# Performance work log

Measured on AMD Instinct MI355X. Metric: run time of the kernel, lower is better.

## Reference

```python
import jax, jax.numpy as jnp
import numpy as np

N_SEGMENTS = 50000  # number of destination nodes (index values in [0, N_SEGMENTS))


def setup_inputs() -> dict:
    key = jax.random.key(0)
    k1, k2 = jax.random.split(key)
    input = jax.random.normal(k1, (1600000, 64), dtype=jnp.float32)
    index = jax.random.randint(k2, (1600000,), 0, N_SEGMENTS, dtype=jnp.int64)
    return {"input": input, "index": index}


def reference(input, index):
    # Sum-aggregate rows of `input` grouped by `index`: out[n] = sum_{e: index[e]==n} input[e]
    # Equivalent to the custom loma_sum_aggr forward (scatter-add segmented reduction).
    return jax.ops.segment_sum(input, index, num_segments=N_SEGMENTS)
```

## Files before the change

kernel.cpp:

```cpp
#include <hip/hip_runtime.h>

#define N_SEGMENTS 50000
#define N_ROWS     1600000
#define N_FEAT     64

__global__ void hist_kernel(const int* __restrict__ idx, int* __restrict__ counts) {
    int i = blockIdx.x * 256 + threadIdx.x;
    if (i < N_ROWS) atomicAdd(&counts[idx[i]], 1);
}

__device__ __forceinline__ int wave_incl_scan(int v) {
    int lane = threadIdx.x & 63;
#pragma unroll
    for (int d = 1; d < 64; d <<= 1) {
        int t = __shfl_up(v, d, 64);
        if (lane >= d) v += t;
    }
    return v;
}

__global__ void scan_kernel(const int* __restrict__ counts,
                            int* __restrict__ seg_start,
                            int* __restrict__ cursor) {
    __shared__ int wave_off[16];
    __shared__ int s_carry;
    const int tid  = threadIdx.x;
    const int lane = tid & 63;
    const int wid  = tid >> 6;
    if (tid == 0) s_carry = 0;
    __syncthreads();

    for (int base = 0; base < N_SEGMENTS; base += 1024) {
        int i = base + tid;
        int v = (i < N_SEGMENTS) ? counts[i] : 0;
        int incl = wave_incl_scan(v);
        if (lane == 63) wave_off[wid] = incl;
        __syncthreads();
        if (wid == 0) {
            int ws    = (lane < 16) ? wave_off[lane] : 0;
            int wincl = wave_incl_scan(ws);
            if (lane < 16) wave_off[lane] = wincl - ws;
        }
        __syncthreads();
        int excl = incl - v + wave_off[wid] + s_carry;
        if (i < N_SEGMENTS) { seg_start[i] = excl; cursor[i] = excl; }
        __syncthreads();
        if (tid == 1023) s_carry = excl + v;
        __syncthreads();
    }
    if (tid == 0) seg_start[N_SEGMENTS] = s_carry;
}

__global__ void scatter_kernel(const int* __restrict__ idx,
                               int* __restrict__ cursor,
                               int* __restrict__ rowids) {
    int i = blockIdx.x * 256 + threadIdx.x;
    if (i < N_ROWS) {
        int s = idx[i];
        int p = atomicAdd(&cursor[s], 1);
        rowids[p] = i;
    }
}

__global__ void __launch_bounds__(256)
reduce_kernel(const float* __restrict__ in,
              const int*   __restrict__ rowids,
              const int*   __restrict__ seg_start,
              float*       __restrict__ out) {
    const int wid  = threadIdx.x >> 6;
    const int lane = threadIdx.x & 63;
    const int seg  = blockIdx.x * 4 + wid;
    if (seg >= N_SEGMENTS) return;

    const int beg = seg_start[seg];
    const int end = seg_start[seg + 1];

    float acc = 0.f;
    int r = beg;
    for (; r + 4 <= end; r += 4) {
        int r0 = rowids[r], r1 = rowids[r + 1], r2 = rowids[r + 2], r3 = rowids[r + 3];
        float v0 = in[(long long)r0 * N_FEAT + lane];
        float v1 = in[(long long)r1 * N_FEAT + lane];
        float v2 = in[(long long)r2 * N_FEAT + lane];
        float v3 = in[(long long)r3 * N_FEAT + lane];
        acc += v0; acc += v1; acc += v2; acc += v3;
    }
    for (; r < end; ++r)
        acc += in[(long long)rowids[r] * N_FEAT + lane];

    out[(long long)seg * N_FEAT + lane] = acc;
}

extern "C" void kernel_launch(void* const* d_in, const int* in_sizes, int n_in,
                              void* d_out, int out_size, void* d_ws, size_t ws_size,
                              hipStream_t stream) {
    const float* in  = (const float*)d_in[0];
    const int*   idx = (const int*)d_in[1];
    float*       out = (float*)d_out;

    int* counts    = (int*)d_ws;
    int* seg_start = counts + 50048;
    int* cursor    = seg_start + 50048;
    int* rowids    = cursor + 50048;

    hipMemsetAsync(counts, 0, N_SEGMENTS * sizeof(int), stream);

    const int ROW_BLOCKS = (N_ROWS + 255) / 256;
    hist_kernel   <<<ROW_BLOCKS, 256, 0, stream>>>(idx, counts);
    scan_kernel   <<<1, 1024, 0, stream>>>(counts, seg_start, cursor);
    scatter_kernel<<<ROW_BLOCKS, 256, 0, stream>>>(idx, cursor, rowids);

    const int SEG_BLOCKS = (N_SEGMENTS + 3) / 4;
    reduce_kernel <<<SEG_BLOCKS, 256, 0, stream>>>(in, rowids, seg_start, out);
}
```

Measured before the change: 786.1 us.

## Parallelize prefix scan across blocks and vectorize segment reduce with float4

Replaces the single-block serial scan over 50000 counts with a three-stage multi-block scan (block sums, mid scan, final offsets). The reduce kernel now has each wave load four rows at once as float4, with 16 lanes per row, and combines the four partial sums with xor shuffles before storing. This targets the serial latency of the scan and the narrow per-lane gather loads, at the cost of two extra kernel launches and more workspace.

```diff
diff --git a/kernel.cpp b/kernel.cpp
--- a/kernel.cpp
+++ b/kernel.cpp
@@ -3,11 +3,7 @@
 #define N_SEGMENTS 50000
 #define N_ROWS     1600000
 #define N_FEAT     64
-
-__global__ void hist_kernel(const int* __restrict__ idx, int* __restrict__ counts) {
-    int i = blockIdx.x * 256 + threadIdx.x;
-    if (i < N_ROWS) atomicAdd(&counts[idx[i]], 1);
-}
+#define SCAN_BLOCKS 196
 
 __device__ __forceinline__ int wave_incl_scan(int v) {
     int lane = threadIdx.x & 63;
@@ -19,36 +15,57 @@
     return v;
 }
 
-__global__ void scan_kernel(const int* __restrict__ counts,
-                            int* __restrict__ seg_start,
-                            int* __restrict__ cursor) {
-    __shared__ int wave_off[16];
-    __shared__ int s_carry;
-    const int tid  = threadIdx.x;
-    const int lane = tid & 63;
-    const int wid  = tid >> 6;
-    if (tid == 0) s_carry = 0;
+__global__ void hist_kernel(const int* __restrict__ idx, int* __restrict__ counts) {
+    int i = blockIdx.x * 256 + threadIdx.x;
+    if (i < N_ROWS) atomicAdd(&counts[idx[i]], 1);
+}
+
+__global__ void scan_sums(const int* __restrict__ counts, int* __restrict__ bsums) {
+    const int lane = threadIdx.x & 63, wid = threadIdx.x >> 6;
+    int i = blockIdx.x * 256 + threadIdx.x;
+    int v = (i < N_SEGMENTS) ? counts[i] : 0;
+#pragma unroll
+    for (int m = 1; m < 64; m <<= 1) v += __shfl_xor(v, m, 64);
+    __shared__ int ws[4];
+    if (lane == 0) ws[wid] = v;
     __syncthreads();
+    if (threadIdx.x == 0) bsums[blockIdx.x] = ws[0] + ws[1] + ws[2] + ws[3];
+}
 
-    for (int base = 0; base < N_SEGMENTS; base += 1024) {
-        int i = base + tid;
-        int v = (i < N_SEGMENTS) ? counts[i] : 0;
-        int incl = wave_incl_scan(v);
-        if (lane == 63) wave_off[wid] = incl;
-        __syncthreads();
-        if (wid == 0) {
-            int ws    = (lane < 16) ? wave_off[lane] : 0;
-            int wincl = wave_incl_scan(ws);
-            if (lane < 16) wave_off[lane] = wincl - ws;
-        }
-        __syncthreads();
-        int excl = incl - v + wave_off[wid] + s_carry;
-        if (i < N_SEGMENTS) { seg_start[i] = excl; cursor[i] = excl; }
-        __syncthreads();
-        if (tid == 1023) s_carry = excl + v;
-        __syncthreads();
+__global__ void scan_mid(const int* __restrict__ bsums, int* __restrict__ boffs) {
+    const int tid = threadIdx.x, lane = tid & 63, wid = tid >> 6;
+    __shared__ int ws[4];
+    int v = (tid < SCAN_BLOCKS) ? bsums[tid] : 0;
+    int incl = wave_incl_scan(v);
+    if (lane == 63) ws[wid] = incl;
+    __syncthreads();
+    if (wid == 0) {
+        int s = (lane < 4) ? ws[lane] : 0;
+        int wincl = wave_incl_scan(s);
+        if (lane < 4) ws[lane] = wincl - s;
     }
-    if (tid == 0) seg_start[N_SEGMENTS] = s_carry;
+    __syncthreads();
+    if (tid < SCAN_BLOCKS) boffs[tid] = incl - v + ws[wid];
+}
+
+__global__ void scan_final(const int* __restrict__ counts, const int* __restrict__ boffs,
+                           int* __restrict__ seg_start, int* __restrict__ cursor) {
+    const int tid = threadIdx.x, lane = tid & 63, wid = tid >> 6;
+    int i = blockIdx.x * 256 + tid;
+    int v = (i < N_SEGMENTS) ? counts[i] : 0;
+    int incl = wave_incl_scan(v);
+    __shared__ int ws[4];
+    if (lane == 63) ws[wid] = incl;
+    __syncthreads();
+    if (wid == 0) {
+        int s = (lane < 4) ? ws[lane] : 0;
+        int wincl = wave_incl_scan(s);
+        if (lane < 4) ws[lane] = wincl - s;
+    }
+    __syncthreads();
+    int excl = incl - v + ws[wid] + boffs[blockIdx.x];
+    if (i < N_SEGMENTS) { seg_start[i] = excl; cursor[i] = excl; }
+    if (blockIdx.x == 0 && tid == 0) seg_start[N_SEGMENTS] = N_ROWS;
 }
 
 __global__ void scatter_kernel(const int* __restrict__ idx,
@@ -56,8 +73,7 @@
                                int* __restrict__ rowids) {
     int i = blockIdx.x * 256 + threadIdx.x;
     if (i < N_ROWS) {
-        int s = idx[i];
-        int p = atomicAdd(&cursor[s], 1);
+        int p = atomicAdd(&cursor[idx[i]], 1);
         rowids[p] = i;
     }
 }
@@ -75,20 +91,49 @@
     const int beg = seg_start[seg];
     const int end = seg_start[seg + 1];
 
-    float acc = 0.f;
+    const int sub = lane >> 4;
+    const int c4  = lane & 15;
+    const float4* in4 = (const float4*)in;
+
+    float4 acc = make_float4(0.f, 0.f, 0.f, 0.f);
+
     int r = beg;
+    for (; r + 16 <= end; r += 16) {
+        int ra = rowids[r +      sub];
+        int rb = rowids[r +  4 + sub];
+        int rc = rowids[r +  8 + sub];
+        int rd = rowids[r + 12 + sub];
+        float4 va = in4[(long long)ra * 16 + c4];
+        float4 vb = in4[(long long)rb * 16 + c4];
+        float4 vc = in4[(long long)rc * 16 + c4];
+        float4 vd = in4[(long long)rd * 16 + c4];
+        acc.x += va.x + vb.x + vc.x + vd.x;
+        acc.y += va.y + vb.y + vc.y + vd.y;
+        acc.z += va.z + vb.z + vc.z + vd.z;
+        acc.w += va.w + vb.w + vc.w + vd.w;
+    }
     for (; r + 4 <= end; r += 4) {
-        int r0 = rowids[r], r1 = rowids[r + 1], r2 = rowids[r + 2], r3 = rowids[r + 3];
-        float v0 = in[(long long)r0 * N_FEAT + lane];
-        float v1 = in[(long long)r1 * N_FEAT + lane];
-        float v2 = in[(long long)r2 * N_FEAT + lane];
-        float v3 = in[(long long)r3 * N_FEAT + lane];
-        acc += v0; acc += v1; acc += v2; acc += v3;
+        int row = rowids[r + sub];
+        float4 v = in4[(long long)row * 16 + c4];
+        acc.x += v.x; acc.y += v.y; acc.z += v.z; acc.w += v.w;
     }
-    for (; r < end; ++r)
-        acc += in[(long long)rowids[r] * N_FEAT + lane];
+    if (r + sub < end) {
+        int row = rowids[r + sub];
+        float4 v = in4[(long long)row * 16 + c4];
+        acc.x += v.x; acc.y += v.y; acc.z += v.z; acc.w += v.w;
+    }
 
-    out[(long long)seg * N_FEAT + lane] = acc;
+#pragma unroll
+    for (int m = 16; m <= 32; m <<= 1) {
+        acc.x += __shfl_xor(acc.x, m, 64);
+        acc.y += __shfl_xor(acc.y, m, 64);
+        acc.z += __shfl_xor(acc.z, m, 64);
+        acc.w += __shfl_xor(acc.w, m, 64);
+    }
+
+    if (sub == 0) {
+        ((float4*)out)[(long long)seg * 16 + c4] = acc;
+    }
 }
 
 extern "C" void kernel_launch(void* const* d_in, const int* in_sizes, int n_in,
@@ -102,12 +147,16 @@
     int* seg_start = counts + 50048;
     int* cursor    = seg_start + 50048;
     int* rowids    = cursor + 50048;
+    int* bsums     = rowids + 1600000;
+    int* boffs     = bsums + 256;
 
     hipMemsetAsync(counts, 0, N_SEGMENTS * sizeof(int), stream);
 
     const int ROW_BLOCKS = (N_ROWS + 255) / 256;
     hist_kernel   <<<ROW_BLOCKS, 256, 0, stream>>>(idx, counts);
-    scan_kernel   <<<1, 1024, 0, stream>>>(counts, seg_start, cursor);
+    scan_sums     <<<SCAN_BLOCKS, 256, 0, stream>>>(counts, bsums);
+    scan_mid      <<<1, 256, 0, stream>>>(bsums, boffs);
+    scan_final    <<<SCAN_BLOCKS, 256, 0, stream>>>(counts, boffs, seg_start, cursor);
     scatter_kernel<<<ROW_BLOCKS, 256, 0, stream>>>(idx, cursor, rowids);
 
     const int SEG_BLOCKS = (N_SEGMENTS + 3) / 4;
```

Measured after the change: 751.8 us. -4.4%, faster.
